# Performance work log

Measured on AMD Instinct MI355X. Metric: run time of the kernel, lower is better.

## Reference

```python
import jax, jax.numpy as jnp
import numpy as np

N = 20000      # nodes
E = 640000     # edges
F_IN = 256     # num_features
HID = 256      # hidden_dim
EMB = 256      # embedding_dim
OUT = 1        # output_dim


def setup_inputs() -> dict:
    key = jax.random.key(0)
    ks = jax.random.split(key, 8)
    g = lambda k, shp: jax.random.normal(k, shp, dtype=jnp.float32) / np.sqrt(shp[0]).astype(np.float32)
    return {
        "x": jax.random.normal(ks[0], (N, F_IN), dtype=jnp.float32),
        "edge_index": jax.random.randint(ks[1], (2, E), 0, N, dtype=jnp.int64),
        "W1": g(ks[2], (F_IN, HID)),
        "b1": jnp.zeros((HID,), jnp.float32),
        "Wh": g(ks[3], (HID, HID)),
        "bh": jnp.zeros((HID,), jnp.float32),
        "W2": g(ks[4], (HID, EMB)),
        "b2": jnp.zeros((EMB,), jnp.float32),
        "Wout": g(ks[5], (EMB, OUT)),
        "bout": jnp.zeros((OUT,), jnp.float32),
    }


def reference(x, edge_index, W1, b1, Wh, bh, W2, b2, Wout, bout):
    n = x.shape[0]
    # PyG GCNConv: add self-loops, symmetric normalization D^-1/2 (A+I) D^-1/2
    loop = jnp.arange(n, dtype=edge_index.dtype)
    row = jnp.concatenate([edge_index[0], loop])  # source j
    col = jnp.concatenate([edge_index[1], loop])  # target i
    deg = jax.ops.segment_sum(jnp.ones(row.shape[0], x.dtype), col, num_segments=n)
    dinv = jnp.where(deg > 0, jax.lax.rsqrt(deg), 0.0)
    norm = dinv[row] * dinv[col]  # [E+N]

    def conv(h, W, b):
        hw = h @ W                                   # dense GEMM [n, d_out]
        msg = hw[row] * norm[:, None]                # gather + scale
        return jax.ops.segment_sum(msg, col, num_segments=n) + b  # scatter-add

    h = jax.nn.relu(conv(x, W1, b1))   # gcn1 (dropout_rate=0 -> identity)
    h = jax.nn.relu(conv(h, Wh, bh))   # hidden GCNConv
    h = conv(h, W2, b2)                # gcn2 -> embedding
    out = h @ Wout + bout              # Decoder_linear
    return (out, h)
```

## Files before the change

### kernel.cpp

```cpp
#include <hip/hip_runtime.h>
#include <hip/hip_bf16.h>

#define NN 20000
#define EE 640000

typedef __attribute__((ext_vector_type(8))) short bf16x8;
typedef __attribute__((ext_vector_type(4))) float f32x4;

__device__ __forceinline__ ushort f2b(float f) {
    __hip_bfloat16 h = __float2bfloat16(f);
    return *(ushort*)&h;
}
__device__ __forceinline__ float b2f(ushort u) {
    __hip_bfloat16 h = *(__hip_bfloat16*)&u;
    return __bfloat162float(h);
}

__device__ __forceinline__ void acc8(float m, bf16x8 v, float* acc) {
    union { bf16x8 v; unsigned u[4]; } t;
    t.v = v;
    #pragma unroll
    for (int k = 0; k < 4; ++k) {
        acc[2 * k]     = fmaf(m, __uint_as_float(t.u[k] << 16), acc[2 * k]);
        acc[2 * k + 1] = fmaf(m, __uint_as_float(t.u[k] & 0xffff0000u), acc[2 * k + 1]);
    }
}

__device__ __forceinline__ void gload16(const ushort* g, ushort* l) {
    __builtin_amdgcn_global_load_lds(
        (const __attribute__((address_space(1))) void*)g,
        (__attribute__((address_space(3))) void*)l, 16, 0, 0);
}


__global__ void init_cnt_kernel(int* __restrict__ cnt, int n) {
    int i = blockIdx.x * 256 + threadIdx.x;
    if (i < n) cnt[i] = 0;
}

__global__ void hist_kernel(const int* __restrict__ col, int* __restrict__ cnt, int e) {
    int i = blockIdx.x * 256 + threadIdx.x;
    if (i < e) atomicAdd(&cnt[col[i]], 1);
}

__device__ __forceinline__ int block_exscan(int v) {
    __shared__ int wsum[4];
    int tid = threadIdx.x, lane = tid & 63, w = tid >> 6;
    int x = v;
    #pragma unroll
    for (int d = 1; d < 64; d <<= 1) {
        int y = __shfl_up(x, d, 64);
        if (lane >= d) x += y;
    }
    if (lane == 63) wsum[w] = x;
    __syncthreads();
    if (tid == 0) {
        int s = 0;
        #pragma unroll
        for (int k = 0; k < 4; ++k) { int t = wsum[k]; wsum[k] = s; s += t; }
    }
    __syncthreads();
    return wsum[w] + x - v;
}

__global__ __launch_bounds__(256) void scan_p1_kernel(const int* __restrict__ cnt,
                                                      int* __restrict__ offs,
                                                      int* __restrict__ bsum,
                                                      float* __restrict__ dinv, int n) {
    int i = blockIdx.x * 256 + threadIdx.x;
    int v = (i < n) ? cnt[i] : 0;
    int e = block_exscan(v);
    if (i < n) {
        offs[i] = e;
        dinv[i] = rsqrtf((float)(v + 1));
    }
    if (threadIdx.x == 255) bsum[blockIdx.x] = e + v;
}

__global__ __launch_bounds__(256) void scan_p2_kernel(int* __restrict__ bsum, int nblk) {
    int t = threadIdx.x;
    int v = (t < nblk) ? bsum[t] : 0;
    int e = block_exscan(v);
    if (t < nblk) bsum[t] = e;
}

__global__ __launch_bounds__(256) void scan_p3_kernel(int* __restrict__ offs,
                                                      const int* __restrict__ bsum,
                                                      int* __restrict__ cursor, int n) {
    int i = blockIdx.x * 256 + threadIdx.x;
    if (i < n) {
        int o = offs[i] + bsum[blockIdx.x];
        offs[i] = o;
        cursor[i] = o;
    }
}

__global__ void scatter_kernel(const int* __restrict__ row, const int* __restrict__ col,
                               const float* __restrict__ dinv, int* __restrict__ cursor,
                               unsigned* __restrict__ pq, int e) {
    int i = blockIdx.x * 256 + threadIdx.x;
    if (i >= e) return;
    int s = row[i], d = col[i];
    int pos = atomicAdd(&cursor[d], 1);
    unsigned nb = f2b(dinv[s] * dinv[d]);
    pq[pos] = (nb << 16) | (unsigned)s;
}

__global__ __launch_bounds__(256) void prep_kernel(
    const float* __restrict__ W1, const float* __restrict__ Wh,
    const float* __restrict__ W2, ushort* __restrict__ Wt,
    const float* __restrict__ x, ushort* __restrict__ xb,
    const float* __restrict__ bout, float* __restrict__ outv, int n) {
    int bid = blockIdx.x;
    if (bid < 768) {
        const float* W = (bid < 256) ? W1 : ((bid < 512) ? Wh : W2);
        ushort* dst = Wt + (size_t)(bid >> 8) * 256 * 512;
        int col = bid & 255;
        #pragma unroll
        for (int kv = threadIdx.x; kv < 512; kv += 256) {
            int k = kv & 255;
            float w = W[(size_t)k * 256 + col];
            ushort hi = f2b(w);
            dst[(size_t)col * 512 + kv] = (kv < 256) ? hi : f2b(w - b2f(hi));
        }
    } else if (bid < 768 + 2500) {
        int i = (bid - 768) * 256 + threadIdx.x;
        if (i < n * 32) {
            float4 a = ((const float4*)x)[2 * i];
            float4 b = ((const float4*)x)[2 * i + 1];
            union { bf16x8 v; ushort s[8]; } o;
            o.s[0] = f2b(a.x); o.s[1] = f2b(a.y); o.s[2] = f2b(a.z); o.s[3] = f2b(a.w);
            o.s[4] = f2b(b.x); o.s[5] = f2b(b.y); o.s[6] = f2b(b.z); o.s[7] = f2b(b.w);
            ((bf16x8*)xb)[i] = o.v;
        }
    } else {
        int i = (bid - 3268) * 256 + threadIdx.x;
        if (i < n) outv[i] = bout[0];
    }
}

__global__ __launch_bounds__(256) void gemm_mfma_kernel(
    const ushort* __restrict__ A, const ushort* __restrict__ Wt,
    ushort* __restrict__ G, int n) {
    __shared__ ushort Ast[2][128][64];
    __shared__ ushort Bst[2][64][64];
    int tid = threadIdx.x;
    int lane = tid & 63, wid = tid >> 6;
    int rowbase = blockIdx.x * 128;
    int colbase = blockIdx.y * 64;

    f32x4 zero = {0.f, 0.f, 0.f, 0.f};
    f32x4 acc[2][4];
    #pragma unroll
    for (int m = 0; m < 2; ++m)
        #pragma unroll
        for (int nn = 0; nn < 4; ++nn) acc[m][nn] = zero;

    int rsub = lane >> 3, sl = lane & 7;
    const ushort* asrc[4];
    #pragma unroll
    for (int q = 0; q < 4; ++q) {
        int rin = wid * 32 + q * 8 + rsub;
        int c = sl ^ (rin & 7);
        int gr = min(rowbase + rin, n - 1);
        asrc[q] = A + (size_t)gr * 256 + c * 8;
    }
    const ushort* bsrc[2];
    #pragma unroll
    for (int q = 0; q < 2; ++q) {
        int rin = wid * 16 + q * 8 + rsub;
        int c = sl ^ (rin & 7);
        bsrc[q] = Wt + (size_t)(colbase + rin) * 512 + c * 8;
    }

    auto stage = [&](int kt, int buf) {
        int kv0 = kt * 64;
        int acol0 = kv0 & 255;
        #pragma unroll
        for (int q = 0; q < 4; ++q)
            gload16(asrc[q] + acol0, &Ast[buf][wid * 32 + q * 8][0]);
        #pragma unroll
        for (int q = 0; q < 2; ++q)
            gload16(bsrc[q] + kv0, &Bst[buf][wid * 16 + q * 8][0]);
    };

    stage(0, 0);
    for (int kt = 0; kt < 8; ++kt) {
        int cur = kt & 1;
        if (kt < 7) {
            stage(kt + 1, cur ^ 1);
            asm volatile("s_waitcnt vmcnt(6)" ::: "memory");
        } else {
            asm volatile("s_waitcnt vmcnt(0)" ::: "memory");
        }
        __builtin_amdgcn_s_barrier();
        #pragma unroll
        for (int kk = 0; kk < 2; ++kk) {
            int clog = kk * 4 + (lane >> 4);
            bf16x8 af[2], bf[4];
            #pragma unroll
            for (int m = 0; m < 2; ++m) {
                int row = wid * 32 + m * 16 + (lane & 15);
                af[m] = *(const bf16x8*)&Ast[cur][row][(clog ^ (row & 7)) * 8];
            }
            #pragma unroll
            for (int nn = 0; nn < 4; ++nn) {
                int row = nn * 16 + (lane & 15);
                bf[nn] = *(const bf16x8*)&Bst[cur][row][(clog ^ (row & 7)) * 8];
            }
            #pragma unroll
            for (int m = 0; m < 2; ++m)
                #pragma unroll
                for (int nn = 0; nn < 4; ++nn)
                    acc[m][nn] = __builtin_amdgcn_mfma_f32_16x16x32_bf16(
                        af[m], bf[nn], acc[m][nn], 0, 0, 0);
        }
        __builtin_amdgcn_s_barrier();
    }

    #pragma unroll
    for (int nn = 0; nn < 4; ++nn) {
        int col = colbase + nn * 16 + (lane & 15);
        #pragma unroll
        for (int m = 0; m < 2; ++m) {
            int grow0 = rowbase + wid * 32 + m * 16 + ((lane >> 4) << 2);
            f32x4 v = acc[m][nn];
            #pragma unroll
            for (int rr = 0; rr < 4; ++rr) {
                int row = grow0 + rr;
                if (row < n)
                    G[(size_t)row * 256 + col] = f2b(v[rr]);
            }
        }
    }
}

template<bool FINAL>
__global__ __launch_bounds__(256) void agg_kernel(
    const ushort* __restrict__ g,
    const int* __restrict__ offs, const int* __restrict__ cnt,
    const unsigned* __restrict__ pq,
    const float* __restrict__ dinv,
    const float* __restrict__ bias,
    ushort* __restrict__ hb,
    float* __restrict__ h3,
    const float* __restrict__ Wout, float* __restrict__ outv,
    int n) {
    int chunk = blockIdx.x & 3;
    int lane = threadIdx.x & 63;
    int half = lane >> 5;
    int esub = (lane >> 3) & 3;
    int fsub = lane & 7;
    int node = (blockIdx.x >> 2) * 8 + (threadIdx.x >> 6) * 2 + half;
    const ushort* base = g + chunk * 64 + fsub * 8;

    int beg = offs[node], num = cnt[node];
    float acc[8] = {};

    unsigned q0 = pq[(esub)      < num ? beg + esub      : 0];
    unsigned q1 = pq[(4 + esub)  < num ? beg + 4 + esub  : 0];
    unsigned q2 = pq[(8 + esub)  < num ? beg + 8 + esub  : 0];
    unsigned q3 = pq[(12 + esub) < num ? beg + 12 + esub : 0];

    for (int j = 0; j < num; j += 16) {
        int jn = j + 16;
        unsigned p0 = pq[(jn + esub)      < num ? beg + jn + esub      : 0];
        unsigned p1 = pq[(jn + 4 + esub)  < num ? beg + jn + 4 + esub  : 0];
        unsigned p2 = pq[(jn + 8 + esub)  < num ? beg + jn + 8 + esub  : 0];
        unsigned p3 = pq[(jn + 12 + esub) < num ? beg + jn + 12 + esub : 0];

        float m0 = (j +      esub) < num ? __uint_as_float(q0 & 0xffff0000u) : 0.f;
        float m1 = (j + 4  + esub) < num ? __uint_as_float(q1 & 0xffff0000u) : 0.f;
        float m2 = (j + 8  + esub) < num ? __uint_as_float(q2 & 0xffff0000u) : 0.f;
        float m3 = (j + 12 + esub) < num ? __uint_as_float(q3 & 0xffff0000u) : 0.f;
        bf16x8 v0 = *(const bf16x8*)(base + (size_t)(q0 & 0xffffu) * 256);
        bf16x8 v1 = *(const bf16x8*)(base + (size_t)(q1 & 0xffffu) * 256);
        bf16x8 v2 = *(const bf16x8*)(base + (size_t)(q2 & 0xffffu) * 256);
        bf16x8 v3 = *(const bf16x8*)(base + (size_t)(q3 & 0xffffu) * 256);
        acc8(m0, v0, acc);
        acc8(m1, v1, acc);
        acc8(m2, v2, acc);
        acc8(m3, v3, acc);
        q0 = p0; q1 = p1; q2 = p2; q3 = p3;
    }

    #pragma unroll
    for (int d = 8; d < 32; d <<= 1)
        #pragma unroll
        for (int k = 0; k < 8; ++k)
            acc[k] += __shfl_xor(acc[k], d, 64);

    if (esub == 0) {
        float di = dinv[node];
        bf16x8 sv = *(const bf16x8*)(base + (size_t)node * 256);
        acc8(di * di, sv, acc);
        int feat = chunk * 64 + fsub * 8;
        float4 b0 = *(const float4*)(bias + feat);
        float4 b1 = *(const float4*)(bias + feat + 4);
        acc[0] += b0.x; acc[1] += b0.y; acc[2] += b0.z; acc[3] += b0.w;
        acc[4] += b1.x; acc[5] += b1.y; acc[6] += b1.z; acc[7] += b1.w;
        if (!FINAL) {
            union { bf16x8 v; ushort s[8]; } o;
            #pragma unroll
            for (int k = 0; k < 8; ++k)
                o.s[k] = f2b(fmaxf(acc[k], 0.f));
            *(bf16x8*)(hb + (size_t)node * 256 + feat) = o.v;
        } else {
            float4 o0 = {acc[0], acc[1], acc[2], acc[3]};
            float4 o1 = {acc[4], acc[5], acc[6], acc[7]};
            *(float4*)(h3 + (size_t)node * 256 + feat)     = o0;
            *(float4*)(h3 + (size_t)node * 256 + feat + 4) = o1;
            float4 w0 = *(const float4*)(Wout + feat);
            float4 w1 = *(const float4*)(Wout + feat + 4);
            float dot = acc[0] * w0.x + acc[1] * w0.y + acc[2] * w0.z + acc[3] * w0.w
                      + acc[4] * w1.x + acc[5] * w1.y + acc[6] * w1.z + acc[7] * w1.w;
            #pragma unroll
            for (int d = 1; d < 8; d <<= 1)
                dot += __shfl_xor(dot, d, 64);
            if (fsub == 0) atomicAdd(&outv[node], dot);
        }
    }
}

extern "C" void kernel_launch(void* const* d_in, const int* in_sizes, int n_in,
                              void* d_out, int out_size, void* d_ws, size_t ws_size,
                              hipStream_t stream) {
    const int n = NN, e = EE;
    const float* x    = (const float*)d_in[0];
    const int*   eidx = (const int*)d_in[1];
    const float* W1   = (const float*)d_in[2];
    const float* b1   = (const float*)d_in[3];
    const float* Wh   = (const float*)d_in[4];
    const float* bh   = (const float*)d_in[5];
    const float* W2   = (const float*)d_in[6];
    const float* b2   = (const float*)d_in[7];
    const float* Wout = (const float*)d_in[8];
    const float* bout = (const float*)d_in[9];
    const int* row = eidx;
    const int* col = eidx + e;

    char* ws = (char*)d_ws;
    int*      cnt     = (int*)ws;      ws += (size_t)n * 4;
    int*      offs    = (int*)ws;      ws += (size_t)n * 4;
    int*      cursor  = (int*)ws;      ws += (size_t)n * 4;
    float*    dinv    = (float*)ws;    ws += (size_t)n * 4;
    int*      bsum    = (int*)ws;      ws += (size_t)256 * 4;
    unsigned* pq      = (unsigned*)ws; ws += (size_t)e * 4;
    ushort*   xb      = (ushort*)ws;   ws += (size_t)n * 256 * 2;
    ushort*   hb      = (ushort*)ws;   ws += (size_t)n * 256 * 2;
    ushort*   g2      = (ushort*)ws;   ws += (size_t)n * 256 * 2;
    ushort*   wt      = (ushort*)ws;   ws += (size_t)3 * 256 * 512 * 2;
    ushort* wt1 = wt;
    ushort* wt2 = wt + (size_t)256 * 512;
    ushort* wt3 = wt + (size_t)2 * 256 * 512;

    float* outv = (float*)d_out;
    float* h3   = (float*)d_out + n;

    int nb_n = (n + 255) / 256;
    int nb_e = (e + 255) / 256;

    init_cnt_kernel<<<nb_n, 256, 0, stream>>>(cnt, n);
    hist_kernel<<<nb_e, 256, 0, stream>>>(col, cnt, e);
    scan_p1_kernel<<<nb_n, 256, 0, stream>>>(cnt, offs, bsum, dinv, n);
    scan_p2_kernel<<<1, 256, 0, stream>>>(bsum, nb_n);
    scan_p3_kernel<<<nb_n, 256, 0, stream>>>(offs, bsum, cursor, n);
    scatter_kernel<<<nb_e, 256, 0, stream>>>(row, col, dinv, cursor, pq, e);

    prep_kernel<<<768 + 2500 + 79, 256, 0, stream>>>(W1, Wh, W2, wt, x, xb, bout, outv, n);

    int agrid = (n / 8) * 4;
    dim3 ggrid((n + 127) / 128, 4);

    gemm_mfma_kernel<<<ggrid, 256, 0, stream>>>(xb, wt1, g2, n);
    agg_kernel<false><<<agrid, 256, 0, stream>>>(
        g2, offs, cnt, pq, dinv, b1, hb, nullptr, nullptr, nullptr, n);
    gemm_mfma_kernel<<<ggrid, 256, 0, stream>>>(hb, wt2, g2, n);
    agg_kernel<false><<<agrid, 256, 0, stream>>>(
        g2, offs, cnt, pq, dinv, bh, hb, nullptr, nullptr, nullptr, n);
    gemm_mfma_kernel<<<ggrid, 256, 0, stream>>>(hb, wt3, g2, n);
    agg_kernel<true><<<agrid, 256, 0, stream>>>(
        g2, offs, cnt, pq, dinv, b2, nullptr, h3, Wout, outv, n);
}
```

Measured before the change: 223.1 us.

## Widen GEMM K-stage to split-K halves and unroll SpMM gather by eight

The GEMM now stages both 256-wide halves of the packed weight (the 512-wide K of Wt) together in one 128-row B tile per K step. It halves the k-loop trip count and issues two MFMAs per accumulator per step, which reduces barrier and loop overhead but doubles B shared memory. The SpMM aggregation loop now keeps eight gathered rows in flight per iteration instead of four. This raises memory-level parallelism at the cost of more registers.

```diff
diff --git a/kernel.cpp b/kernel.cpp
--- a/kernel.cpp
+++ b/kernel.cpp
@@ -143,7 +143,7 @@
     const ushort* __restrict__ A, const ushort* __restrict__ Wt,
     ushort* __restrict__ G, int n) {
     __shared__ ushort Ast[2][128][64];
-    __shared__ ushort Bst[2][64][64];
+    __shared__ ushort Bst[2][128][64];
     int tid = threadIdx.x;
     int lane = tid & 63, wid = tid >> 6;
     int rowbase = blockIdx.x * 128;
@@ -158,38 +158,34 @@
 
     int rsub = lane >> 3, sl = lane & 7;
     const ushort* asrc[4];
+    const ushort* bsrc[4];
     #pragma unroll
     for (int q = 0; q < 4; ++q) {
         int rin = wid * 32 + q * 8 + rsub;
         int c = sl ^ (rin & 7);
         int gr = min(rowbase + rin, n - 1);
         asrc[q] = A + (size_t)gr * 256 + c * 8;
-    }
-    const ushort* bsrc[2];
-    #pragma unroll
-    for (int q = 0; q < 2; ++q) {
-        int rin = wid * 16 + q * 8 + rsub;
-        int c = sl ^ (rin & 7);
-        bsrc[q] = Wt + (size_t)(colbase + rin) * 512 + c * 8;
+        int col_r = rin & 63;
+        int part = rin >> 6;
+        bsrc[q] = Wt + (size_t)(colbase + col_r) * 512 + part * 256 + c * 8;
     }
 
     auto stage = [&](int kt, int buf) {
         int kv0 = kt * 64;
-        int acol0 = kv0 & 255;
         #pragma unroll
         for (int q = 0; q < 4; ++q)
-            gload16(asrc[q] + acol0, &Ast[buf][wid * 32 + q * 8][0]);
-        #pragma unroll
-        for (int q = 0; q < 2; ++q)
-            gload16(bsrc[q] + kv0, &Bst[buf][wid * 16 + q * 8][0]);
+            gload16(asrc[q] + kv0, &Ast[buf][wid * 32 + q * 8][0]);
+        #pragma unroll
+        for (int q = 0; q < 4; ++q)
+            gload16(bsrc[q] + kv0, &Bst[buf][wid * 32 + q * 8][0]);
     };
 
     stage(0, 0);
-    for (int kt = 0; kt < 8; ++kt) {
+    for (int kt = 0; kt < 4; ++kt) {
         int cur = kt & 1;
-        if (kt < 7) {
+        if (kt < 3) {
             stage(kt + 1, cur ^ 1);
-            asm volatile("s_waitcnt vmcnt(6)" ::: "memory");
+            asm volatile("s_waitcnt vmcnt(8)" ::: "memory");
         } else {
             asm volatile("s_waitcnt vmcnt(0)" ::: "memory");
         }
@@ -197,7 +193,7 @@
         #pragma unroll
         for (int kk = 0; kk < 2; ++kk) {
             int clog = kk * 4 + (lane >> 4);
-            bf16x8 af[2], bf[4];
+            bf16x8 af[2], bfh[4], bfl[4];
             #pragma unroll
             for (int m = 0; m < 2; ++m) {
                 int row = wid * 32 + m * 16 + (lane & 15);
@@ -205,15 +201,20 @@
             }
             #pragma unroll
             for (int nn = 0; nn < 4; ++nn) {
-                int row = nn * 16 + (lane & 15);
-                bf[nn] = *(const bf16x8*)&Bst[cur][row][(clog ^ (row & 7)) * 8];
+                int rowh = nn * 16 + (lane & 15);
+                int rowl = rowh + 64;
+                bfh[nn] = *(const bf16x8*)&Bst[cur][rowh][(clog ^ (rowh & 7)) * 8];
+                bfl[nn] = *(const bf16x8*)&Bst[cur][rowl][(clog ^ (rowl & 7)) * 8];
             }
             #pragma unroll
             for (int m = 0; m < 2; ++m)
                 #pragma unroll
-                for (int nn = 0; nn < 4; ++nn)
+                for (int nn = 0; nn < 4; ++nn) {
                     acc[m][nn] = __builtin_amdgcn_mfma_f32_16x16x32_bf16(
-                        af[m], bf[nn], acc[m][nn], 0, 0, 0);
+                        af[m], bfh[nn], acc[m][nn], 0, 0, 0);
+                    acc[m][nn] = __builtin_amdgcn_mfma_f32_16x16x32_bf16(
+                        af[m], bfl[nn], acc[m][nn], 0, 0, 0);
+                }
         }
         __builtin_amdgcn_s_barrier();
     }
@@ -257,31 +258,31 @@
     int beg = offs[node], num = cnt[node];
     float acc[8] = {};
 
-    unsigned q0 = pq[(esub)      < num ? beg + esub      : 0];
-    unsigned q1 = pq[(4 + esub)  < num ? beg + 4 + esub  : 0];
-    unsigned q2 = pq[(8 + esub)  < num ? beg + 8 + esub  : 0];
-    unsigned q3 = pq[(12 + esub) < num ? beg + 12 + esub : 0];
-
-    for (int j = 0; j < num; j += 16) {
-        int jn = j + 16;
-        unsigned p0 = pq[(jn + esub)      < num ? beg + jn + esub      : 0];
-        unsigned p1 = pq[(jn + 4 + esub)  < num ? beg + jn + 4 + esub  : 0];
-        unsigned p2 = pq[(jn + 8 + esub)  < num ? beg + jn + 8 + esub  : 0];
-        unsigned p3 = pq[(jn + 12 + esub) < num ? beg + jn + 12 + esub : 0];
-
-        float m0 = (j +      esub) < num ? __uint_as_float(q0 & 0xffff0000u) : 0.f;
-        float m1 = (j + 4  + esub) < num ? __uint_as_float(q1 & 0xffff0000u) : 0.f;
-        float m2 = (j + 8  + esub) < num ? __uint_as_float(q2 & 0xffff0000u) : 0.f;
-        float m3 = (j + 12 + esub) < num ? __uint_as_float(q3 & 0xffff0000u) : 0.f;
-        bf16x8 v0 = *(const bf16x8*)(base + (size_t)(q0 & 0xffffu) * 256);
-        bf16x8 v1 = *(const bf16x8*)(base + (size_t)(q1 & 0xffffu) * 256);
-        bf16x8 v2 = *(const bf16x8*)(base + (size_t)(q2 & 0xffffu) * 256);
-        bf16x8 v3 = *(const bf16x8*)(base + (size_t)(q3 & 0xffffu) * 256);
-        acc8(m0, v0, acc);
-        acc8(m1, v1, acc);
-        acc8(m2, v2, acc);
-        acc8(m3, v3, acc);
-        q0 = p0; q1 = p1; q2 = p2; q3 = p3;
+    unsigned q[8];
+    #pragma unroll
+    for (int u = 0; u < 8; ++u) {
+        int i = u * 4 + esub;
+        q[u] = pq[i < num ? beg + i : 0];
+    }
+
+    for (int j = 0; j < num; j += 32) {
+        bf16x8 v[8];
+        #pragma unroll
+        for (int u = 0; u < 8; ++u)
+            v[u] = *(const bf16x8*)(base + (size_t)(q[u] & 0xffffu) * 256);
+        unsigned p[8];
+        #pragma unroll
+        for (int u = 0; u < 8; ++u) {
+            int i = j + 32 + u * 4 + esub;
+            p[u] = pq[i < num ? beg + i : 0];
+        }
+        #pragma unroll
+        for (int u = 0; u < 8; ++u) {
+            float m = (j + u * 4 + esub) < num ? __uint_as_float(q[u] & 0xffff0000u) : 0.f;
+            acc8(m, v[u], acc);
+        }
+        #pragma unroll
+        for (int u = 0; u < 8; ++u) q[u] = p[u];
     }
 
     #pragma unroll
```

Result: slower. 236.4 us (+5.9%).
